# Kernel optimization log

Hardware: AMD Instinct MI355X
Metric: run time of the kernel (lower is better)

The kernel has to match this reference:

```python
import jax, jax.numpy as jnp
import numpy as np

N = 8192
EMB = 256
NHID = 64
ALPHA = 0.2  # LeakyReLU negative slope
NEG_INF = -9e15


def setup_inputs() -> dict:
    key = jax.random.key(0)
    k1, k2, k3, k4 = jax.random.split(key, 4)
    inp = jax.random.normal(k1, (N, EMB), dtype=jnp.float32)
    adj = jax.random.randint(k2, (N, N), 0, 2, dtype=jnp.int32)
    W = jax.random.normal(k3, (EMB, NHID), dtype=jnp.float32) * 0.05
    a = jax.random.normal(k4, (2 * NHID,), dtype=jnp.float32) * 0.05
    return {"input": inp, "adj": adj, "W": W, "a": a}


def reference(input, adj, W, a):
    # h = W(input): [N, nhid]
    h = input @ W
    # e_ij = leakyrelu(h_i . a[:nhid] + h_j . a[nhid:])  (equiv. to concat-pairs @ a)
    s_src = h @ a[:NHID]   # [N]
    s_dst = h @ a[NHID:]   # [N]
    e = jax.nn.leaky_relu(s_src[:, None] + s_dst[None, :], ALPHA)  # [N, N]
    attention = jnp.where(adj > 0, e, NEG_INF)
    attention = jax.nn.softmax(attention, axis=1)
    # edge dropout p=0.0 (eval) -> identity
    h_prime = attention @ h  # [N, nhid]
    return h_prime
```

## Files before the change

### kernel.cpp

```cpp
#include <hip/hip_runtime.h>
#include <hip/hip_bf16.h>

#define N_NODES 8192
#define EMB 256
#define NHID 64
#define LOG2E 1.44269504088896340736f
#define S_SPLIT 32
#define COLS 256
#define NKT 8
#define HROWB 264

typedef __attribute__((ext_vector_type(8))) short bf16x8;
typedef __attribute__((ext_vector_type(4))) float f32x4;

static __device__ __forceinline__ short f2bf(float f) {
  __hip_bfloat16 h = __float2bfloat16(f);
  return *reinterpret_cast<short*>(&h);
}

static __device__ __forceinline__ short f2bf_fast(float f) {
  unsigned u = __builtin_bit_cast(unsigned, f);
  return (short)((u + 0x8000u) >> 16);
}

__global__ __launch_bounds__(256) void gat_k1(
    const float* __restrict__ in, const float* __restrict__ W,
    const float* __restrict__ a, short* __restrict__ hT,
    float* __restrict__ ssrc, float* __restrict__ sdst) {
  int wave = threadIdx.x >> 6, lane = threadIdx.x & 63;
  int row = blockIdx.x * 4 + wave;
  int d = lane;
  const float4* in4 = reinterpret_cast<const float4*>(in + (size_t)row * EMB);
  float acc = 0.f;
#pragma unroll 4
  for (int k4 = 0; k4 < EMB / 4; ++k4) {
    float4 x = in4[k4];
    int k = k4 * 4;
    acc = fmaf(x.x, W[(k + 0) * NHID + d], acc);
    acc = fmaf(x.y, W[(k + 1) * NHID + d], acc);
    acc = fmaf(x.z, W[(k + 2) * NHID + d], acc);
    acc = fmaf(x.w, W[(k + 3) * NHID + d], acc);
  }
  hT[(size_t)d * N_NODES + row] = f2bf(acc);
  float p1 = acc * a[d];
  float p2 = acc * a[NHID + d];
#pragma unroll
  for (int off = 32; off > 0; off >>= 1) {
    p1 += __shfl_xor(p1, off);
    p2 += __shfl_xor(p2, off);
  }
  if (lane == 0) {
    ssrc[row] = p1 * LOG2E;
    sdst[row] = p2 * LOG2E;
  }
}

__global__ __launch_bounds__(256, 4) void gat_k2(
    const int* __restrict__ adj, const short* __restrict__ hT,
    const float* __restrict__ ssrc, const float* __restrict__ sdst,
    float* __restrict__ pacc, float* __restrict__ pz) {
  __shared__ short hlds[64 * HROWB];
  __shared__ float tlds[COLS];

  int split = blockIdx.x >> 7;
  int rb = blockIdx.x & 127;
  int tid = threadIdx.x;
  int c0 = split * COLS;

#pragma unroll
  for (int p = 0; p < 8; ++p) {
    int flat = p * 4096 + tid * 16;
    int srow = flat >> 9;
    int scol = (flat & 511) >> 1;
    bf16x8 v = *reinterpret_cast<const bf16x8*>(
        hT + (size_t)srow * N_NODES + c0 + scol);
    *reinterpret_cast<bf16x8*>(&hlds[srow * HROWB + scol]) = v;
  }
  if (tid < 64) {
    float4 tv4 = *reinterpret_cast<const float4*>(sdst + c0 + tid * 4);
    *reinterpret_cast<float4*>(&tlds[tid * 4]) = tv4;
  }
  __syncthreads();

  int wv = tid >> 6, lane = tid & 63;
  int lrow = lane & 15, kg = lane >> 4;
  int r0 = rb * 64 + wv * 16;
  int row = r0 + lrow;
  float s_i = ssrc[row];
  const int* adjr = adj + (size_t)row * N_NODES + c0 + kg * 8;

  f32x4 acc0 = {0.f, 0.f, 0.f, 0.f};
  f32x4 acc1 = acc0, acc2 = acc0, acc3 = acc0;
  float zacc = 0.f;

  int4 rgA[3], rgB[3];
#pragma unroll
  for (int i = 0; i < 3; ++i) {
    rgA[i] = *reinterpret_cast<const int4*>(adjr + i * 32);
    rgB[i] = *reinterpret_cast<const int4*>(adjr + i * 32 + 4);
  }

#pragma unroll
  for (int kt = 0; kt < NKT; ++kt) {
    int rs = kt % 3;
    int4 ca = rgA[rs], cb = rgB[rs];
    if (kt + 3 < NKT) {
      rgA[rs] = *reinterpret_cast<const int4*>(adjr + (kt + 3) * 32);
      rgB[rs] = *reinterpret_cast<const int4*>(adjr + (kt + 3) * 32 + 4);
    }
    int cbase = kt * 32 + kg * 8;
    float4 tA = *reinterpret_cast<const float4*>(&tlds[cbase]);
    float4 tB = *reinterpret_cast<const float4*>(&tlds[cbase + 4]);
    bf16x8 b0 = *reinterpret_cast<const bf16x8*>(&hlds[(lrow + 0) * HROWB + cbase]);
    bf16x8 b1 = *reinterpret_cast<const bf16x8*>(&hlds[(lrow + 16) * HROWB + cbase]);
    bf16x8 b2 = *reinterpret_cast<const bf16x8*>(&hlds[(lrow + 32) * HROWB + cbase]);
    bf16x8 b3 = *reinterpret_cast<const bf16x8*>(&hlds[(lrow + 48) * HROWB + cbase]);

    float tv[8] = {tA.x, tA.y, tA.z, tA.w, tB.x, tB.y, tB.z, tB.w};
    int av[8] = {ca.x, ca.y, ca.z, ca.w, cb.x, cb.y, cb.z, cb.w};
    bf16x8 af;
#pragma unroll
    for (int e = 0; e < 8; ++e) {
      float x = s_i + tv[e];
      float lk = fmaxf(x, 0.2f * x);
      float ev = __builtin_amdgcn_exp2f(lk);
      float w = (av[e] != 0) ? ev : 0.f;
      zacc += w;
      af[e] = f2bf_fast(w);
    }
    acc0 = __builtin_amdgcn_mfma_f32_16x16x32_bf16(af, b0, acc0, 0, 0, 0);
    acc1 = __builtin_amdgcn_mfma_f32_16x16x32_bf16(af, b1, acc1, 0, 0, 0);
    acc2 = __builtin_amdgcn_mfma_f32_16x16x32_bf16(af, b2, acc2, 0, 0, 0);
    acc3 = __builtin_amdgcn_mfma_f32_16x16x32_bf16(af, b3, acc3, 0, 0, 0);
  }

  float z = zacc;
  z += __shfl_xor(z, 16);
  z += __shfl_xor(z, 32);
  if (lane < 16) pz[(size_t)split * N_NODES + r0 + lane] = z;

  float* pa = pacc + (size_t)split * (N_NODES * NHID);
#pragma unroll
  for (int reg = 0; reg < 4; ++reg) {
    int orow = r0 + kg * 4 + reg;
    pa[(size_t)orow * NHID + 0 * 16 + lrow] = acc0[reg];
    pa[(size_t)orow * NHID + 1 * 16 + lrow] = acc1[reg];
    pa[(size_t)orow * NHID + 2 * 16 + lrow] = acc2[reg];
    pa[(size_t)orow * NHID + 3 * 16 + lrow] = acc3[reg];
  }
}

__global__ __launch_bounds__(256) void gat_k3(
    const float* __restrict__ pacc, const float* __restrict__ pz,
    float* __restrict__ out) {
  int idx = blockIdx.x * 256 + threadIdx.x;
  int row = idx >> 6;
  float num = 0.f, den = 0.f;
#pragma unroll 8
  for (int s = 0; s < S_SPLIT; ++s) {
    num += pacc[(size_t)s * (N_NODES * NHID) + idx];
    den += pz[(size_t)s * N_NODES + row];
  }
  out[idx] = num / den;
}

extern "C" void kernel_launch(void* const* d_in, const int* in_sizes, int n_in,
                              void* d_out, int out_size, void* d_ws, size_t ws_size,
                              hipStream_t stream) {
  (void)in_sizes; (void)n_in; (void)out_size; (void)ws_size;
  const float* in = (const float*)d_in[0];
  const int* adj = (const int*)d_in[1];
  const float* W = (const float*)d_in[2];
  const float* a = (const float*)d_in[3];
  float* out = (float*)d_out;

  char* w = (char*)d_ws;
  short* hT = (short*)w;
  float* ssrc = (float*)(w + (1u << 20));
  float* sdst = ssrc + N_NODES;
  float* pz = sdst + N_NODES;
  float* pacc = pz + (size_t)S_SPLIT * N_NODES;

  gat_k1<<<N_NODES / 4, 256, 0, stream>>>(in, W, a, hT, ssrc, sdst);
  gat_k2<<<128 * S_SPLIT, 256, 0, stream>>>(adj, hT, ssrc, sdst, pacc, pz);
  gat_k3<<<(N_NODES * NHID) / 256, 256, 0, stream>>>(pacc, pz, out);
}
```

Before: 449.0 us.

## Stage adjacency tile as LDS bitmask with coalesced loads; vectorize reduction kernel

The attention kernel no longer streams adjacency ints per lane from 16 different rows inside the MFMA loop. Before the barrier, each wave cooperatively loads contiguous row segments of the adjacency tile, packs each group of 8 ints into a byte mask, and stores it in LDS. The inner loop then reads one mask byte per step. The final split-reduction kernel is also changed to use float4 loads and stores with a reciprocal multiply. The trade-off is that the previous register-level prefetch, which overlapped adjacency loads with compute, is gone, so the whole adjacency tile is loaded before any math starts.

Result: faster. 419.1 us (-6.7%).

```diff
diff --git a/kernel.cpp b/kernel.cpp
--- a/kernel.cpp
+++ b/kernel.cpp
@@ -8,7 +8,8 @@
 #define S_SPLIT 32
 #define COLS 256
 #define NKT 8
-#define HROWB 264
+#define HROW 264
+#define MROW 36
 
 typedef __attribute__((ext_vector_type(8))) short bf16x8;
 typedef __attribute__((ext_vector_type(4))) float f32x4;
@@ -59,13 +60,15 @@
     const int* __restrict__ adj, const short* __restrict__ hT,
     const float* __restrict__ ssrc, const float* __restrict__ sdst,
     float* __restrict__ pacc, float* __restrict__ pz) {
-  __shared__ short hlds[64 * HROWB];
+  __shared__ short hlds[64 * HROW];
+  __shared__ unsigned char mlds[64 * MROW];
   __shared__ float tlds[COLS];
 
   int split = blockIdx.x >> 7;
   int rb = blockIdx.x & 127;
   int tid = threadIdx.x;
   int c0 = split * COLS;
+  int wv = tid >> 6, lane = tid & 63;
 
 #pragma unroll
   for (int p = 0; p < 8; ++p) {
@@ -74,57 +77,56 @@
     int scol = (flat & 511) >> 1;
     bf16x8 v = *reinterpret_cast<const bf16x8*>(
         hT + (size_t)srow * N_NODES + c0 + scol);
-    *reinterpret_cast<bf16x8*>(&hlds[srow * HROWB + scol]) = v;
+    *reinterpret_cast<bf16x8*>(&hlds[srow * HROW + scol]) = v;
   }
   if (tid < 64) {
-    float4 tv4 = *reinterpret_cast<const float4*>(sdst + c0 + tid * 4);
-    *reinterpret_cast<float4*>(&tlds[tid * 4]) = tv4;
+    float4 t4 = *reinterpret_cast<const float4*>(sdst + c0 + tid * 4);
+    *reinterpret_cast<float4*>(&tlds[tid * 4]) = t4;
+  }
+  {
+    int h = lane >> 5, sl = lane & 31;
+#pragma unroll
+    for (int p = 0; p < 8; ++p) {
+      int r = wv * 16 + p * 2 + h;
+      const int* ap = adj + (size_t)(rb * 64 + r) * N_NODES + c0 + sl * 8;
+      int4 v0 = *reinterpret_cast<const int4*>(ap);
+      int4 v1 = *reinterpret_cast<const int4*>(ap + 4);
+      unsigned b = (unsigned)(v0.x != 0) | ((unsigned)(v0.y != 0) << 1) |
+                   ((unsigned)(v0.z != 0) << 2) | ((unsigned)(v0.w != 0) << 3) |
+                   ((unsigned)(v1.x != 0) << 4) | ((unsigned)(v1.y != 0) << 5) |
+                   ((unsigned)(v1.z != 0) << 6) | ((unsigned)(v1.w != 0) << 7);
+      mlds[r * MROW + sl] = (unsigned char)b;
+    }
   }
   __syncthreads();
 
-  int wv = tid >> 6, lane = tid & 63;
   int lrow = lane & 15, kg = lane >> 4;
   int r0 = rb * 64 + wv * 16;
-  int row = r0 + lrow;
-  float s_i = ssrc[row];
-  const int* adjr = adj + (size_t)row * N_NODES + c0 + kg * 8;
+  float s_i = ssrc[r0 + lrow];
 
   f32x4 acc0 = {0.f, 0.f, 0.f, 0.f};
   f32x4 acc1 = acc0, acc2 = acc0, acc3 = acc0;
   float zacc = 0.f;
 
-  int4 rgA[3], rgB[3];
-#pragma unroll
-  for (int i = 0; i < 3; ++i) {
-    rgA[i] = *reinterpret_cast<const int4*>(adjr + i * 32);
-    rgB[i] = *reinterpret_cast<const int4*>(adjr + i * 32 + 4);
-  }
-
 #pragma unroll
   for (int kt = 0; kt < NKT; ++kt) {
-    int rs = kt % 3;
-    int4 ca = rgA[rs], cb = rgB[rs];
-    if (kt + 3 < NKT) {
-      rgA[rs] = *reinterpret_cast<const int4*>(adjr + (kt + 3) * 32);
-      rgB[rs] = *reinterpret_cast<const int4*>(adjr + (kt + 3) * 32 + 4);
-    }
-    int cbase = kt * 32 + kg * 8;
-    float4 tA = *reinterpret_cast<const float4*>(&tlds[cbase]);
-    float4 tB = *reinterpret_cast<const float4*>(&tlds[cbase + 4]);
-    bf16x8 b0 = *reinterpret_cast<const bf16x8*>(&hlds[(lrow + 0) * HROWB + cbase]);
-    bf16x8 b1 = *reinterpret_cast<const bf16x8*>(&hlds[(lrow + 16) * HROWB + cbase]);
-    bf16x8 b2 = *reinterpret_cast<const bf16x8*>(&hlds[(lrow + 32) * HROWB + cbase]);
-    bf16x8 b3 = *reinterpret_cast<const bf16x8*>(&hlds[(lrow + 48) * HROWB + cbase]);
+    int cb = kt * 32 + kg * 8;
+    unsigned mb = mlds[(wv * 16 + lrow) * MROW + kt * 4 + kg];
+    float4 tA = *reinterpret_cast<const float4*>(&tlds[cb]);
+    float4 tB = *reinterpret_cast<const float4*>(&tlds[cb + 4]);
+    bf16x8 b0 = *reinterpret_cast<const bf16x8*>(&hlds[(lrow + 0) * HROW + cb]);
+    bf16x8 b1 = *reinterpret_cast<const bf16x8*>(&hlds[(lrow + 16) * HROW + cb]);
+    bf16x8 b2 = *reinterpret_cast<const bf16x8*>(&hlds[(lrow + 32) * HROW + cb]);
+    bf16x8 b3 = *reinterpret_cast<const bf16x8*>(&hlds[(lrow + 48) * HROW + cb]);
 
     float tv[8] = {tA.x, tA.y, tA.z, tA.w, tB.x, tB.y, tB.z, tB.w};
-    int av[8] = {ca.x, ca.y, ca.z, ca.w, cb.x, cb.y, cb.z, cb.w};
     bf16x8 af;
 #pragma unroll
     for (int e = 0; e < 8; ++e) {
       float x = s_i + tv[e];
       float lk = fmaxf(x, 0.2f * x);
       float ev = __builtin_amdgcn_exp2f(lk);
-      float w = (av[e] != 0) ? ev : 0.f;
+      float w = (mb & (1u << e)) ? ev : 0.f;
       zacc += w;
       af[e] = f2bf_fast(w);
     }
@@ -153,15 +155,20 @@
 __global__ __launch_bounds__(256) void gat_k3(
     const float* __restrict__ pacc, const float* __restrict__ pz,
     float* __restrict__ out) {
-  int idx = blockIdx.x * 256 + threadIdx.x;
-  int row = idx >> 6;
-  float num = 0.f, den = 0.f;
+  int t = blockIdx.x * 256 + threadIdx.x;
+  int row = t >> 4;
+  float4 num = {0.f, 0.f, 0.f, 0.f};
+  float den = 0.f;
 #pragma unroll 8
   for (int s = 0; s < S_SPLIT; ++s) {
-    num += pacc[(size_t)s * (N_NODES * NHID) + idx];
+    float4 p = *reinterpret_cast<const float4*>(
+        &pacc[(size_t)s * (N_NODES * NHID) + (size_t)t * 4]);
+    num.x += p.x; num.y += p.y; num.z += p.z; num.w += p.w;
     den += pz[(size_t)s * N_NODES + row];
   }
-  out[idx] = num / den;
+  float r = 1.f / den;
+  float4 o = {num.x * r, num.y * r, num.z * r, num.w * r};
+  *reinterpret_cast<float4*>(&out[(size_t)t * 4]) = o;
 }
 
 extern "C" void kernel_launch(void* const* d_in, const int* in_sizes, int n_in,
@@ -183,5 +190,5 @@
 
   gat_k1<<<N_NODES / 4, 256, 0, stream>>>(in, W, a, hT, ssrc, sdst);
   gat_k2<<<128 * S_SPLIT, 256, 0, stream>>>(adj, hT, ssrc, sdst, pacc, pz);
-  gat_k3<<<(N_NODES * NHID) / 256, 256, 0, stream>>>(pacc, pz, out);
+  gat_k3<<<(N_NODES * NHID) / (256 * 4), 256, 0, stream>>>(pacc, pz, out);
 }
```
